# Optimization experiments

Hardware: AMD Instinct MI355X
Metric: run time of the kernel (lower is better)

The kernel has to match this reference:

```python
import jax, jax.numpy as jnp
import numpy as np
import math

VOCAB, E, CTX, DK, DH, H, HID, L = 50257, 768, 2048, 64, 64, 12, 3072, 2
B, S = 2, 2048
NEG_INF = -1e30


def _pos_encoding(seq_len, dim):
    pos = jnp.arange(seq_len, dtype=jnp.float32)[:, None]
    i = jnp.arange(dim, dtype=jnp.float32)[None, :]
    angle = pos / jnp.power(10000.0, 2.0 * i / dim)
    return jnp.where(jnp.arange(dim)[None, :] % 2 == 0, jnp.sin(angle), jnp.cos(angle))


def _layernorm(x, scale, bias, eps=1e-5):
    mu = jnp.mean(x, axis=-1, keepdims=True)
    var = jnp.var(x, axis=-1, keepdims=True)
    return (x - mu) * jax.lax.rsqrt(var + eps) * scale + bias


def setup_inputs() -> dict:
    key = jax.random.key(0)
    ks = jax.random.split(key, 10)
    s = 0.02  # init scale for stability
    return {
        "tokens": jax.random.randint(ks[0], (B, S), 0, VOCAB),
        "emb": jax.random.normal(ks[1], (VOCAB, E), jnp.float32) * s,
        "ln1_s": jnp.ones((L, E), jnp.float32),
        "ln1_b": jnp.zeros((L, E), jnp.float32),
        "Wq": jax.random.normal(ks[2], (L, H, E, DK), jnp.float32) * s,
        "bq": jnp.zeros((L, H, DK), jnp.float32),
        "Wk": jax.random.normal(ks[3], (L, H, E, DK), jnp.float32) * s,
        "bk": jnp.zeros((L, H, DK), jnp.float32),
        "Wv": jax.random.normal(ks[4], (L, H, E, DH), jnp.float32) * s,
        "bv": jnp.zeros((L, H, DH), jnp.float32),
        "ln2_s": jnp.ones((L, E), jnp.float32),
        "ln2_b": jnp.zeros((L, E), jnp.float32),
        "W1": jax.random.normal(ks[5], (L, E, HID), jnp.float32) * s,
        "b1": jnp.zeros((L, HID), jnp.float32),
        "W2": jax.random.normal(ks[6], (L, HID, E), jnp.float32) * s,
        "b2": jnp.zeros((L, E), jnp.float32),
        "Wout": jax.random.normal(ks[7], (E, VOCAB), jnp.float32) * s,
        "bout": jnp.zeros((VOCAB,), jnp.float32),
    }


def reference(tokens, emb, ln1_s, ln1_b, Wq, bq, Wk, bk, Wv, bv, ln2_s, ln2_b, W1, b1, W2, b2, Wout, bout):
    seq = tokens.shape[1]
    x = emb[tokens] + _pos_encoding(seq, E)  # [B,S,E]
    causal = jnp.triu(jnp.full((seq, seq), NEG_INF, jnp.float32), k=1)
    for l in range(Wq.shape[0]):
        # pre-norm on attention input; note residual adds to the NORMALIZED h (faithful to original)
        h = _layernorm(x, ln1_s[l], ln1_b[l])
        q = jnp.einsum('bse,hed->bhsd', h, Wq[l]) + bq[l][None, :, None, :]
        k = jnp.einsum('bse,hed->bhsd', h, Wk[l]) + bk[l][None, :, None, :]
        v = jnp.einsum('bse,hed->bhsd', h, Wv[l]) + bv[l][None, :, None, :]
        scores = jnp.einsum('bhsd,bhtd->bhst', q, k) / math.sqrt(DK) + causal
        w = jax.nn.softmax(scores, axis=-1)  # [B,H,S,S]
        o = jnp.einsum('bhst,bhtd->bhsd', w, v)  # [B,H,S,DH]
        o = jnp.transpose(o, (0, 2, 1, 3)).reshape(o.shape[0], seq, H * DH)  # concat heads
        x = h + o
        h2 = _layernorm(x, ln2_s[l], ln2_b[l])
        x = h2 + jnp.einsum('bsf,fe->bse', jax.nn.relu(jnp.einsum('bse,ef->bsf', h2, W1[l]) + b1[l]), W2[l]) + b2[l]
    logits = jnp.einsum('bse,ev->bsv', x, Wout) + bout  # training-mode output
    return logits
```

## Files before the change

kernel.cpp:

```cpp
#include <hip/hip_runtime.h>
#include <stdint.h>

#define DEV static __device__ __forceinline__

typedef unsigned short u16;
typedef __attribute__((ext_vector_type(8))) short short8;
typedef __attribute__((ext_vector_type(4))) float f32x4;

#define B_     2
#define S_     2048
#define E_     768
#define H_     12
#define L_     2
#define HID_   3072
#define VOCAB_ 50257
#define VPAD_  50304
#define M_     4096
#define NQKV_  2304

DEV u16 f2bf(float f) {
  union { float f; unsigned u; } x; x.f = f;
  unsigned r = x.u + 0x7fffu + ((x.u >> 16) & 1u);
  return (u16)(r >> 16);
}

DEV void gload16(const void* g, void* lds) {
  __builtin_amdgcn_global_load_lds(
      (const __attribute__((address_space(1))) unsigned int*)g,
      (__attribute__((address_space(3))) unsigned int*)lds, 16, 0, 0);
}

__global__ __launch_bounds__(256) void k_transp(
    const float* __restrict__ in, u16* __restrict__ out,
    int R, int Cin, long long ib1, long long ib2, long long ob1, long long ob2, int zdiv)
{
  __shared__ float t[32][33];
  const int z = blockIdx.z;
  const float* ib = in  + (size_t)(z / zdiv) * ib1 + (size_t)(z % zdiv) * ib2;
  u16*         ob = out + (size_t)(z / zdiv) * ob1 + (size_t)(z % zdiv) * ob2;
  const int c0 = blockIdx.x * 32, r0 = blockIdx.y * 32;
  const int tx = threadIdx.x, ty = threadIdx.y;
#pragma unroll
  for (int i = 0; i < 4; i++) {
    const int c = c0 + tx, r = r0 + ty + i * 8;
    t[ty + i * 8][tx] = (c < Cin) ? ib[(size_t)r * Cin + c] : 0.f;
  }
  __syncthreads();
#pragma unroll
  for (int i = 0; i < 4; i++) {
    const int orow = c0 + ty + i * 8;
    ob[(size_t)orow * R + r0 + tx] = f2bf(t[tx][ty + i * 8]);
  }
}

__global__ __launch_bounds__(256) void k_pack_bias(
    const float* __restrict__ bq, const float* __restrict__ bk,
    const float* __restrict__ bv, float* __restrict__ bqkv)
{
  const int i = blockIdx.x * 256 + threadIdx.x;
  if (i >= L_ * NQKV_) return;
  const int l = i / NQKV_, n = i % NQKV_;
  const float* s = (n < 768) ? bq : (n < 1536) ? bk : bv;
  bqkv[i] = s[l * 768 + (n % 768)];
}

__global__ __launch_bounds__(256) void k_embed(
    const int* __restrict__ tok, const float* __restrict__ emb, float* __restrict__ x)
{
  const int idx = blockIdx.x * 256 + threadIdx.x;
  const int e = idx % E_;
  const int row = idx / E_;
  const int s = row & (S_ - 1);
  const int t = tok[row];
  const float ang = (float)s * expf((float)e * (-2.0f / 768.f) * 9.210340371976184f);
  const float pe = (e & 1) ? cosf(ang) : sinf(ang);
  x[idx] = emb[(size_t)t * E_ + e] + pe;
}

__global__ __launch_bounds__(256) void k_ln(
    const float* __restrict__ xin, const float* __restrict__ sc,
    const float* __restrict__ bi, float* __restrict__ hout, u16* __restrict__ hb)
{
  const int row  = blockIdx.x * 4 + (threadIdx.x >> 6);
  const int lane = threadIdx.x & 63;
  const float* xr = xin + (size_t)row * E_;
  float v[12];
  float s = 0.f;
#pragma unroll
  for (int i = 0; i < 12; i++) { v[i] = xr[i * 64 + lane]; s += v[i]; }
#pragma unroll
  for (int o = 1; o < 64; o <<= 1) s += __shfl_xor(s, o);
  const float mu = s * (1.f / 768.f);
  float s2 = 0.f;
#pragma unroll
  for (int i = 0; i < 12; i++) { const float d = v[i] - mu; s2 += d * d; }
#pragma unroll
  for (int o = 1; o < 64; o <<= 1) s2 += __shfl_xor(s2, o);
  const float rs = rsqrtf(s2 * (1.f / 768.f) + 1e-5f);
#pragma unroll
  for (int i = 0; i < 12; i++) {
    const int c = i * 64 + lane;
    const float ov = (v[i] - mu) * rs * sc[c] + bi[c];
    hout[(size_t)row * E_ + c] = ov;
    hb[(size_t)row * E_ + c]   = f2bf(ov);
  }
}

__global__ __launch_bounds__(256) void k_f2b(
    const float* __restrict__ in, u16* __restrict__ o, int n)
{
  const int i = blockIdx.x * 256 + threadIdx.x;
  if (i < n) o[i] = f2bf(in[i]);
}

template <int EPI>
__global__ __launch_bounds__(256) void k_gemm(
    const u16* __restrict__ A, const u16* __restrict__ Bt,
    const float* __restrict__ bias, const float* __restrict__ res,
    void* __restrict__ outp, int Mm, int Nn, int Kk, int nreal)
{
  __shared__ __align__(16) u16 As[128 * 32];
  __shared__ __align__(16) u16 Bs[128 * 32];
  const int tid  = threadIdx.x;
  const int lane = tid & 63;
  const int wid  = tid >> 6;
  const int wr = wid >> 1, wc = wid & 1;
  const int m0 = blockIdx.y * 128, n0 = blockIdx.x * 128;

  const u16* Ab = A  + (size_t)m0 * Kk;
  const u16* Bb = Bt + (size_t)n0 * Kk;

  f32x4 acc[4][4];
#pragma unroll
  for (int i = 0; i < 4; i++)
#pragma unroll
    for (int j = 0; j < 4; j++) acc[i][j] = (f32x4){0.f, 0.f, 0.f, 0.f};

  const int c0 = tid, c1 = 256 + tid;
  const int a0row = c0 >> 2, a0k = (c0 & 3) * 8;
  const int a1row = c1 >> 2, a1k = (c1 & 3) * 8;
  const int nk = Kk >> 5;
  const int kg = (lane >> 4) * 8;
  const int arow = wr * 64 + (lane & 15);
  const int brow = wc * 64 + (lane & 15);

  for (int kt = 0; kt < nk; ++kt) {
    const int kof = kt * 32;
    __syncthreads();
    gload16(Ab + (size_t)a0row * Kk + kof + a0k, &As[c0 * 8]);
    gload16(Ab + (size_t)a1row * Kk + kof + a1k, &As[c1 * 8]);
    gload16(Bb + (size_t)a0row * Kk + kof + a0k, &Bs[c0 * 8]);
    gload16(Bb + (size_t)a1row * Kk + kof + a1k, &Bs[c1 * 8]);
    asm volatile("s_waitcnt vmcnt(0)" ::: "memory");
    __syncthreads();
    short8 af[4], bf[4];
#pragma unroll
    for (int i = 0; i < 4; i++) af[i] = *(const short8*)&As[(arow + i * 16) * 32 + kg];
#pragma unroll
    for (int i = 0; i < 4; i++) bf[i] = *(const short8*)&Bs[(brow + i * 16) * 32 + kg];
#pragma unroll
    for (int mi = 0; mi < 4; mi++)
#pragma unroll
      for (int ni = 0; ni < 4; ni++)
        acc[mi][ni] = __builtin_amdgcn_mfma_f32_16x16x32_bf16(af[mi], bf[ni], acc[mi][ni], 0, 0, 0);
  }

  const int colg = lane & 15;
  const int rowg = (lane >> 4) * 4;
#pragma unroll
  for (int mi = 0; mi < 4; mi++) {
#pragma unroll
    for (int ni = 0; ni < 4; ni++) {
      const int col = n0 + wc * 64 + ni * 16 + colg;
      const float bb = (EPI == 3 && col >= nreal) ? 0.f : bias[col];
#pragma unroll
      for (int r = 0; r < 4; r++) {
        const int row = m0 + wr * 64 + mi * 16 + rowg + r;
        float v = acc[mi][ni][r] + bb;
        if (EPI == 0)      ((u16*)outp)[(size_t)row * Nn + col] = f2bf(v);
        else if (EPI == 1) ((u16*)outp)[(size_t)row * Nn + col] = f2bf(fmaxf(v, 0.f));
        else if (EPI == 2) ((float*)outp)[(size_t)row * Nn + col] = v + res[(size_t)row * Nn + col];
        else { if (col < nreal) ((float*)outp)[(size_t)row * nreal + col] = v; }
      }
    }
  }
}

__global__ __launch_bounds__(256) void k_attn(
    const u16* __restrict__ qkv, const float* __restrict__ h, float* __restrict__ x)
{
  const int tid = threadIdx.x, lane = tid & 63, wid = tid >> 6;
  const int bh = blockIdx.y, b = bh / H_, hh = bh % H_;
  const int q0 = blockIdx.x * 64;
  const int qw = q0 + wid * 16;

  __shared__ __align__(16) u16 Ks[32 * 72];
  __shared__ __align__(16) u16 Vt[64 * 40];
  __shared__ __align__(16) u16 Ps[4][16 * 40];

  const size_t rowbase = (size_t)b * S_;
  const u16* qb = qkv + rowbase * NQKV_ + hh * 64;
  const u16* kb = qb + 768;
  const u16* vb = qb + 1536;

  const int l15 = lane & 15;
  const int kg  = (lane >> 4) * 8;

  short8 qf0, qf1;
  {
    const u16* g = qb + (size_t)(qw + l15) * NQKV_ + kg;
    qf0 = *(const short8*)g;
    qf1 = *(const short8*)(g + 32);
  }

  f32x4 ov[4];
#pragma unroll
  for (int i = 0; i < 4; i++) ov[i] = (f32x4){0.f, 0.f, 0.f, 0.f};
  float mr[4], lr[4];
#pragma unroll
  for (int r = 0; r < 4; r++) { mr[r] = -1e30f; lr[r] = 0.f; }

  const int srow = tid >> 3, sc8 = (tid & 7) * 8;
  const int nkt = q0 / 32 + 2;
  for (int kt = 0; kt < nkt; ++kt) {
    __syncthreads();
    {
      const size_t gr = (size_t)(kt * 32 + srow) * NQKV_;
      const uint4 kd = *(const uint4*)(kb + gr + sc8);
      *(uint4*)&Ks[srow * 72 + sc8] = kd;
      const uint4 vd = *(const uint4*)(vb + gr + sc8);
      const u16* ve = (const u16*)&vd;
#pragma unroll
      for (int j = 0; j < 8; j++) Vt[(sc8 + j) * 40 + srow] = ve[j];
    }
    __syncthreads();
    if (kt * 32 <= qw + 15) {
      f32x4 s0 = (f32x4){0.f, 0.f, 0.f, 0.f}, s1 = (f32x4){0.f, 0.f, 0.f, 0.f};
      const short8 k00 = *(const short8*)&Ks[l15 * 72 + kg];
      const short8 k01 = *(const short8*)&Ks[l15 * 72 + 32 + kg];
      const short8 k10 = *(const short8*)&Ks[(16 + l15) * 72 + kg];
      const short8 k11 = *(const short8*)&Ks[(16 + l15) * 72 + 32 + kg];
      s0 = __builtin_amdgcn_mfma_f32_16x16x32_bf16(qf0, k00, s0, 0, 0, 0);
      s0 = __builtin_amdgcn_mfma_f32_16x16x32_bf16(qf1, k01, s0, 0, 0, 0);
      s1 = __builtin_amdgcn_mfma_f32_16x16x32_bf16(qf0, k10, s1, 0, 0, 0);
      s1 = __builtin_amdgcn_mfma_f32_16x16x32_bf16(qf1, k11, s1, 0, 0, 0);

      const int qrow0 = qw + (lane >> 4) * 4;
      const int kc0 = kt * 32 + l15, kc1 = kc0 + 16;
      float p0[4], p1[4], mt[4];
#pragma unroll
      for (int r = 0; r < 4; r++) {
        const int qr = qrow0 + r;
        p0[r] = (kc0 <= qr) ? s0[r] * 0.125f : -1e30f;
        p1[r] = (kc1 <= qr) ? s1[r] * 0.125f : -1e30f;
        mt[r] = fmaxf(p0[r], p1[r]);
      }
#pragma unroll
      for (int r = 0; r < 4; r++) {
#pragma unroll
        for (int off = 1; off < 16; off <<= 1) mt[r] = fmaxf(mt[r], __shfl_xor(mt[r], off));
      }
      float al[4];
#pragma unroll
      for (int r = 0; r < 4; r++) {
        const float mn = fmaxf(mr[r], mt[r]);
        al[r] = __expf(mr[r] - mn);
        mr[r] = mn;
        p0[r] = __expf(p0[r] - mn);
        p1[r] = __expf(p1[r] - mn);
      }
      float ps[4];
#pragma unroll
      for (int r = 0; r < 4; r++) ps[r] = p0[r] + p1[r];
#pragma unroll
      for (int r = 0; r < 4; r++) {
#pragma unroll
        for (int off = 1; off < 16; off <<= 1) ps[r] += __shfl_xor(ps[r], off);
        lr[r] = lr[r] * al[r] + ps[r];
      }
#pragma unroll
      for (int dt = 0; dt < 4; dt++)
#pragma unroll
        for (int r = 0; r < 4; r++) ov[dt][r] *= al[r];

      u16* pw = &Ps[wid][0];
#pragma unroll
      for (int r = 0; r < 4; r++) {
        const int pr = (lane >> 4) * 4 + r;
        pw[pr * 40 + l15]      = f2bf(p0[r]);
        pw[pr * 40 + 16 + l15] = f2bf(p1[r]);
      }
      const short8 pa = *(const short8*)&pw[l15 * 40 + kg];
#pragma unroll
      for (int dt = 0; dt < 4; dt++) {
        const short8 vf = *(const short8*)&Vt[(dt * 16 + l15) * 40 + kg];
        ov[dt] = __builtin_amdgcn_mfma_f32_16x16x32_bf16(pa, vf, ov[dt], 0, 0, 0);
      }
    }
  }
#pragma unroll
  for (int dt = 0; dt < 4; dt++) {
#pragma unroll
    for (int r = 0; r < 4; r++) {
      const int qr = qw + (lane >> 4) * 4 + r;
      const int col = hh * 64 + dt * 16 + l15;
      const size_t idx = (rowbase + qr) * (size_t)E_ + col;
      x[idx] = h[idx] + ov[dt][r] / lr[r];
    }
  }
}

extern "C" void kernel_launch(void* const* d_in, const int* in_sizes, int n_in,
                              void* d_out, int out_size, void* d_ws, size_t ws_size,
                              hipStream_t stream)
{
  const int*   tok  = (const int*)  d_in[0];
  const float* emb  = (const float*)d_in[1];
  const float* ln1s = (const float*)d_in[2];
  const float* ln1b = (const float*)d_in[3];
  const float* Wq   = (const float*)d_in[4];
  const float* bq   = (const float*)d_in[5];
  const float* Wk   = (const float*)d_in[6];
  const float* bk   = (const float*)d_in[7];
  const float* Wv   = (const float*)d_in[8];
  const float* bv   = (const float*)d_in[9];
  const float* ln2s = (const float*)d_in[10];
  const float* ln2b = (const float*)d_in[11];
  const float* W1   = (const float*)d_in[12];
  const float* b1   = (const float*)d_in[13];
  const float* W2   = (const float*)d_in[14];
  const float* b2   = (const float*)d_in[15];
  const float* Wo   = (const float*)d_in[16];
  const float* bo   = (const float*)d_in[17];
  float* out = (float*)d_out;

  char* p = (char*)d_ws;
  float* xf    = (float*)p; p += (size_t)M_ * E_ * 4;
  float* hf    = (float*)p; p += (size_t)M_ * E_ * 4;
  u16*   hb    = (u16*)p;   p += (size_t)M_ * E_ * 2;
  u16*   xb    = (u16*)p;   p += (size_t)M_ * E_ * 2;
  u16*   midb  = (u16*)p;   p += (size_t)M_ * HID_ * 2;
  u16*   qkvb  = (u16*)p;   p += (size_t)M_ * NQKV_ * 2;
  u16*   Wqkvt = (u16*)p;   p += (size_t)L_ * NQKV_ * E_ * 2;
  u16*   W1t   = (u16*)p;   p += (size_t)L_ * HID_ * E_ * 2;
  u16*   W2t   = (u16*)p;   p += (size_t)L_ * E_ * HID_ * 2;
  u16*   Wot   = (u16*)p;   p += (size_t)VPAD_ * E_ * 2;
  float* bqkv  = (float*)p; p += (size_t)L_ * NQKV_ * 4;

  const dim3 tb32(32, 8, 1);
  k_transp<<<dim3(HID_ / 32, E_ / 32, L_), tb32, 0, stream>>>(
      W1, W1t, E_, HID_, (long long)E_ * HID_, 0, (long long)HID_ * E_, 0, 1);
  k_transp<<<dim3(E_ / 32, HID_ / 32, L_), tb32, 0, stream>>>(
      W2, W2t, HID_, E_, (long long)HID_ * E_, 0, (long long)E_ * HID_, 0, 1);
  k_transp<<<dim3(VPAD_ / 32, E_ / 32, 1), tb32, 0, stream>>>(
      Wo, Wot, E_, VOCAB_, 0, 0, 0, 0, 1);
  k_transp<<<dim3(2, E_ / 32, L_ * H_), tb32, 0, stream>>>(
      Wq, Wqkvt, E_, 64, (long long)H_ * E_ * 64, (long long)E_ * 64,
      (long long)NQKV_ * E_, 64LL * E_, H_);
  k_transp<<<dim3(2, E_ / 32, L_ * H_), tb32, 0, stream>>>(
      Wk, Wqkvt + 768 * E_, E_, 64, (long long)H_ * E_ * 64, (long long)E_ * 64,
      (long long)NQKV_ * E_, 64LL * E_, H_);
  k_transp<<<dim3(2, E_ / 32, L_ * H_), tb32, 0, stream>>>(
      Wv, Wqkvt + 1536 * E_, E_, 64, (long long)H_ * E_ * 64, (long long)E_ * 64,
      (long long)NQKV_ * E_, 64LL * E_, H_);
  k_pack_bias<<<18, 256, 0, stream>>>(bq, bk, bv, bqkv);
  k_embed<<<(M_ * E_) / 256, 256, 0, stream>>>(tok, emb, xf);

  for (int l = 0; l < L_; ++l) {
    k_ln<<<M_ / 4, 256, 0, stream>>>(xf, ln1s + l * E_, ln1b + l * E_, hf, hb);
    k_gemm<0><<<dim3(NQKV_ / 128, M_ / 128), 256, 0, stream>>>(
        hb, Wqkvt + (size_t)l * NQKV_ * E_, bqkv + l * NQKV_, nullptr, qkvb, M_, NQKV_, E_, 0);
    k_attn<<<dim3(S_ / 64, B_ * H_), 256, 0, stream>>>(qkvb, hf, xf);
    k_ln<<<M_ / 4, 256, 0, stream>>>(xf, ln2s + l * E_, ln2b + l * E_, hf, hb);
    k_gemm<1><<<dim3(HID_ / 128, M_ / 128), 256, 0, stream>>>(
        hb, W1t + (size_t)l * HID_ * E_, b1 + l * HID_, nullptr, midb, M_, HID_, E_, 0);
    k_gemm<2><<<dim3(E_ / 128, M_ / 128), 256, 0, stream>>>(
        midb, W2t + (size_t)l * E_ * HID_, b2 + l * E_, hf, xf, M_, E_, HID_, 0);
  }
  k_f2b<<<(M_ * E_) / 256, 256, 0, stream>>>(xf, xb, M_ * E_);
  k_gemm<3><<<dim3(VPAD_ / 128, M_ / 128), 256, 0, stream>>>(
      xb, Wot, bo, nullptr, out, M_, VPAD_, E_, VOCAB_);
}
```

Baseline: 1.357 ms.

## Add 256x256-tile 512-thread GEMM with 4-stage async LDS pipeline for wide projections

Introduces a new GEMM kernel with 256x256 output tiles, 8 waves, XOR-swizzled LDS, a 4-deep global_load_lds ring buffer with explicit vmcnt waits, and XCD-aware block remapping. It is used for the QKV, FFN1 and vocabulary projections. The vocabulary padding is raised to a multiple of 256 to fit the new tile. The aim is more data reuse per tile and better overlap of loads with MFMA, at the cost of high register use and one workgroup per CU. The QKV grid of 144 blocks may leave some CUs idle.

```diff
diff --git a/kernel.cpp b/kernel.cpp
--- a/kernel.cpp
+++ b/kernel.cpp
@@ -14,7 +14,7 @@
 #define L_     2
 #define HID_   3072
 #define VOCAB_ 50257
-#define VPAD_  50304
+#define VPAD_  50432
 #define M_     4096
 #define NQKV_  2304
 
@@ -172,7 +172,7 @@
 #pragma unroll
     for (int ni = 0; ni < 4; ni++) {
       const int col = n0 + wc * 64 + ni * 16 + colg;
-      const float bb = (EPI == 3 && col >= nreal) ? 0.f : bias[col];
+      const float bb = bias[col];
 #pragma unroll
       for (int r = 0; r < 4; r++) {
         const int row = m0 + wr * 64 + mi * 16 + rowg + r;
@@ -180,6 +180,112 @@
         if (EPI == 0)      ((u16*)outp)[(size_t)row * Nn + col] = f2bf(v);
         else if (EPI == 1) ((u16*)outp)[(size_t)row * Nn + col] = f2bf(fmaxf(v, 0.f));
         else if (EPI == 2) ((float*)outp)[(size_t)row * Nn + col] = v + res[(size_t)row * Nn + col];
+      }
+    }
+  }
+}
+
+template <int EPI>
+__global__ __launch_bounds__(512, 1) void k_gemm8(
+    const u16* __restrict__ A, const u16* __restrict__ Bt,
+    const float* __restrict__ bias, void* __restrict__ outp,
+    int Nn, int Kk, int nreal)
+{
+  __shared__ __align__(16) u16 As[4][256 * 32];
+  __shared__ __align__(16) u16 Bs[4][256 * 32];
+
+  const int nwg = gridDim.x, cpx = nwg >> 3;
+  int wg = blockIdx.x;
+  wg = (wg & 7) * cpx + (wg >> 3);
+  const int mi = wg & 15, ni = wg >> 4;
+  const int m0 = mi * 256, n0 = ni * 256;
+
+  const int tid = threadIdx.x;
+  const int lane = tid & 63;
+  const int w = tid >> 6;
+  const int wr = w >> 2, wcn = w & 3;
+
+  const u16* Ab = A  + (size_t)m0 * Kk;
+  const u16* Bb = Bt + (size_t)n0 * Kk;
+
+  const int srow = lane >> 2;
+  const int sslot = ((lane & 3) ^ ((lane >> 3) & 3)) * 8;
+  const size_t sA0 = (size_t)(w * 16 + srow) * Kk + sslot;
+  const size_t sA1 = (size_t)((w + 8) * 16 + srow) * Kk + sslot;
+
+  const int l15 = lane & 15, ks = lane >> 4;
+  const int ra0 = wr * 128 + l15;
+  const int aoffb = ra0 * 32 + ((ks ^ ((ra0 >> 1) & 3)) * 8);
+  const int rb0 = wcn * 64 + l15;
+  const int boffb = rb0 * 32 + ((ks ^ ((rb0 >> 1) & 3)) * 8);
+
+  f32x4 acc[8][4];
+#pragma unroll
+  for (int i = 0; i < 8; i++)
+#pragma unroll
+    for (int j = 0; j < 4; j++) acc[i][j] = (f32x4){0.f, 0.f, 0.f, 0.f};
+
+  const int nk = Kk >> 5;
+#pragma unroll
+  for (int t = 0; t < 3; ++t) {
+    const int ko = t * 32;
+    gload16(Ab + sA0 + ko, &As[t][w * 512]);
+    gload16(Ab + sA1 + ko, &As[t][(w + 8) * 512]);
+    gload16(Bb + sA0 + ko, &Bs[t][w * 512]);
+    gload16(Bb + sA1 + ko, &Bs[t][(w + 8) * 512]);
+  }
+
+  for (int t = 0; t < nk; ++t) {
+    const int cur = t & 3;
+    if (t + 3 < nk) {
+      const int nb = (t + 3) & 3;
+      const int ko = (t + 3) * 32;
+      gload16(Ab + sA0 + ko, &As[nb][w * 512]);
+      gload16(Ab + sA1 + ko, &As[nb][(w + 8) * 512]);
+      gload16(Bb + sA0 + ko, &Bs[nb][w * 512]);
+      gload16(Bb + sA1 + ko, &Bs[nb][(w + 8) * 512]);
+      asm volatile("s_waitcnt vmcnt(12)" ::: "memory");
+    } else if (t + 2 < nk) {
+      asm volatile("s_waitcnt vmcnt(8)" ::: "memory");
+    } else if (t + 1 < nk) {
+      asm volatile("s_waitcnt vmcnt(4)" ::: "memory");
+    } else {
+      asm volatile("s_waitcnt vmcnt(0)" ::: "memory");
+    }
+    __builtin_amdgcn_sched_barrier(0);
+    __builtin_amdgcn_s_barrier();
+    __builtin_amdgcn_sched_barrier(0);
+
+    short8 bfr[4];
+#pragma unroll
+    for (int fn = 0; fn < 4; fn++) bfr[fn] = *(const short8*)&Bs[cur][boffb + fn * 512];
+    __builtin_amdgcn_s_setprio(1);
+#pragma unroll
+    for (int fm = 0; fm < 8; fm++) {
+      const short8 af = *(const short8*)&As[cur][aoffb + fm * 512];
+#pragma unroll
+      for (int fn = 0; fn < 4; fn++)
+        acc[fm][fn] = __builtin_amdgcn_mfma_f32_16x16x32_bf16(af, bfr[fn], acc[fm][fn], 0, 0, 0);
+    }
+    __builtin_amdgcn_s_setprio(0);
+    __builtin_amdgcn_sched_barrier(0);
+    __builtin_amdgcn_s_barrier();
+    __builtin_amdgcn_sched_barrier(0);
+  }
+
+  const int rowg = (lane >> 4) * 4;
+#pragma unroll
+  for (int fn = 0; fn < 4; fn++) {
+    const int col = n0 + wcn * 64 + fn * 16 + l15;
+    const float bb = (EPI == 3 && col >= nreal) ? 0.f : bias[col];
+#pragma unroll
+    for (int fm = 0; fm < 8; fm++) {
+#pragma unroll
+      for (int r = 0; r < 4; r++) {
+        const int row = m0 + wr * 128 + fm * 16 + rowg + r;
+        float v = acc[fm][fn][r] + bb;
+        if (EPI == 0)      ((u16*)outp)[(size_t)row * Nn + col] = f2bf(v);
+        else if (EPI == 1) ((u16*)outp)[(size_t)row * Nn + col] = f2bf(fmaxf(v, 0.f));
         else { if (col < nreal) ((float*)outp)[(size_t)row * nreal + col] = v; }
       }
     }
@@ -368,16 +474,16 @@
 
   for (int l = 0; l < L_; ++l) {
     k_ln<<<M_ / 4, 256, 0, stream>>>(xf, ln1s + l * E_, ln1b + l * E_, hf, hb);
-    k_gemm<0><<<dim3(NQKV_ / 128, M_ / 128), 256, 0, stream>>>(
-        hb, Wqkvt + (size_t)l * NQKV_ * E_, bqkv + l * NQKV_, nullptr, qkvb, M_, NQKV_, E_, 0);
+    k_gemm8<0><<<16 * (NQKV_ / 256), 512, 0, stream>>>(
+        hb, Wqkvt + (size_t)l * NQKV_ * E_, bqkv + l * NQKV_, qkvb, NQKV_, E_, 0);
     k_attn<<<dim3(S_ / 64, B_ * H_), 256, 0, stream>>>(qkvb, hf, xf);
     k_ln<<<M_ / 4, 256, 0, stream>>>(xf, ln2s + l * E_, ln2b + l * E_, hf, hb);
-    k_gemm<1><<<dim3(HID_ / 128, M_ / 128), 256, 0, stream>>>(
-        hb, W1t + (size_t)l * HID_ * E_, b1 + l * HID_, nullptr, midb, M_, HID_, E_, 0);
+    k_gemm8<1><<<16 * (HID_ / 256), 512, 0, stream>>>(
+        hb, W1t + (size_t)l * HID_ * E_, b1 + l * HID_, midb, HID_, E_, 0);
     k_gemm<2><<<dim3(E_ / 128, M_ / 128), 256, 0, stream>>>(
         midb, W2t + (size_t)l * E_ * HID_, b2 + l * E_, hf, xf, M_, E_, HID_, 0);
   }
   k_f2b<<<(M_ * E_) / 256, 256, 0, stream>>>(xf, xb, M_ * E_);
-  k_gemm<3><<<dim3(VPAD_ / 128, M_ / 128), 256, 0, stream>>>(
-      xb, Wot, bo, nullptr, out, M_, VPAD_, E_, VOCAB_);
-}
+  k_gemm8<3><<<16 * (VPAD_ / 256), 512, 0, stream>>>(
+      xb, Wot, bo, out, VPAD_, E_, VOCAB_);
+}
```

New measurement: 1.662 ms. +22.5%, slower.

## Add 256x256 pipelined GEMM for vocab projection and fuse bf16 cast into FFN

Applied to the files above, without the earlier changes.

Replaces the 128x128 output-projection GEMM with a new 256x256-tile, 512-thread kernel. It uses K=64 double-buffered LDS staging through direct global-to-LDS loads, an XOR-swizzled LDS layout, MFMA priority hints and an XCD-aware block mapping. The vocab padding grows to a multiple of 256. The last layer's W2 GEMM now also writes the bf16 copy of x, which removes the separate f32-to-bf16 conversion kernel. The goal is higher MFMA utilisation and data reuse on the dominant logits GEMM, at the cost of a more fragile hand-scheduled pipeline, more padded columns, and fewer resident blocks from the larger LDS footprint.

```diff
diff --git a/kernel.cpp b/kernel.cpp
--- a/kernel.cpp
+++ b/kernel.cpp
@@ -14,7 +14,7 @@
 #define L_     2
 #define HID_   3072
 #define VOCAB_ 50257
-#define VPAD_  50304
+#define VPAD_  50432
 #define M_     4096
 #define NQKV_  2304
 
@@ -106,18 +106,11 @@
   }
 }
 
-__global__ __launch_bounds__(256) void k_f2b(
-    const float* __restrict__ in, u16* __restrict__ o, int n)
-{
-  const int i = blockIdx.x * 256 + threadIdx.x;
-  if (i < n) o[i] = f2bf(in[i]);
-}
-
 template <int EPI>
 __global__ __launch_bounds__(256) void k_gemm(
     const u16* __restrict__ A, const u16* __restrict__ Bt,
     const float* __restrict__ bias, const float* __restrict__ res,
-    void* __restrict__ outp, int Mm, int Nn, int Kk, int nreal)
+    void* __restrict__ outp, u16* __restrict__ out2, int Mm, int Nn, int Kk)
 {
   __shared__ __align__(16) u16 As[128 * 32];
   __shared__ __align__(16) u16 Bs[128 * 32];
@@ -172,7 +165,7 @@
 #pragma unroll
     for (int ni = 0; ni < 4; ni++) {
       const int col = n0 + wc * 64 + ni * 16 + colg;
-      const float bb = (EPI == 3 && col >= nreal) ? 0.f : bias[col];
+      const float bb = bias[col];
 #pragma unroll
       for (int r = 0; r < 4; r++) {
         const int row = m0 + wr * 64 + mi * 16 + rowg + r;
@@ -180,7 +173,136 @@
         if (EPI == 0)      ((u16*)outp)[(size_t)row * Nn + col] = f2bf(v);
         else if (EPI == 1) ((u16*)outp)[(size_t)row * Nn + col] = f2bf(fmaxf(v, 0.f));
         else if (EPI == 2) ((float*)outp)[(size_t)row * Nn + col] = v + res[(size_t)row * Nn + col];
-        else { if (col < nreal) ((float*)outp)[(size_t)row * nreal + col] = v; }
+        else if (EPI == 4) {
+          const float o = v + res[(size_t)row * Nn + col];
+          ((float*)outp)[(size_t)row * Nn + col] = o;
+          out2[(size_t)row * Nn + col] = f2bf(o);
+        }
+      }
+    }
+  }
+}
+
+__global__ __launch_bounds__(512, 2) void k_gemm256(
+    const u16* __restrict__ A, const u16* __restrict__ Bt,
+    const float* __restrict__ bias, float* __restrict__ out,
+    int Nn, int Kk, int nreal, int mpx)
+{
+  __shared__ __align__(16) u16 As[2][256 * 64];
+  __shared__ __align__(16) u16 Bs[2][256 * 64];
+
+  const int id = blockIdx.x;
+  const int xcd = id & 7;
+  const int j = id >> 3;
+  const int m0 = (xcd * mpx + (j % mpx)) * 256;
+  const int n0 = (j / mpx) * 256;
+
+  const int tid = threadIdx.x, lane = tid & 63, w = tid >> 6;
+  const int wr = w >> 2, wcn = w & 3;
+  const int l15 = lane & 15, ks = lane >> 4;
+
+  const u16* Ab = A  + (size_t)m0 * Kk;
+  const u16* Bb = Bt + (size_t)n0 * Kk;
+
+  const int srow  = lane >> 3;
+  const int sslot = ((lane & 7) ^ srow) * 8;
+  const int wrow  = w * 8;
+
+  f32x4 acc[8][4];
+#pragma unroll
+  for (int i = 0; i < 8; i++)
+#pragma unroll
+    for (int n = 0; n < 4; n++) acc[i][n] = (f32x4){0.f, 0.f, 0.f, 0.f};
+
+  const int nk = Kk >> 6;
+
+  auto stA = [&](int b, int R, int ko) {
+    gload16(Ab + (size_t)(R + wrow + srow) * Kk + ko + sslot,      &As[b][(R + wrow) * 64]);
+    gload16(Ab + (size_t)(R + 64 + wrow + srow) * Kk + ko + sslot, &As[b][(R + 64 + wrow) * 64]);
+  };
+  auto stB = [&](int b, int R, int ko) {
+    gload16(Bb + (size_t)(R + wrow + srow) * Kk + ko + sslot,      &Bs[b][(R + wrow) * 64]);
+    gload16(Bb + (size_t)(R + 64 + wrow + srow) * Kk + ko + sslot, &Bs[b][(R + 64 + wrow) * 64]);
+  };
+
+  short8 af[4], bf[4];
+  auto ldA = [&](int b, int fmh, int ksub) {
+#pragma unroll
+    for (int i = 0; i < 4; i++) {
+      const int r = wr * 128 + fmh * 64 + i * 16 + l15;
+      const int sl = ((ksub * 4 + ks) ^ (r & 7)) * 8;
+      af[i] = *(const short8*)&As[b][r * 64 + sl];
+    }
+  };
+  auto ldB = [&](int b, int ksub) {
+#pragma unroll
+    for (int n = 0; n < 4; n++) {
+      const int r = wcn * 64 + n * 16 + l15;
+      const int sl = ((ksub * 4 + ks) ^ (r & 7)) * 8;
+      bf[n] = *(const short8*)&Bs[b][r * 64 + sl];
+    }
+  };
+  auto mm = [&](int fmh) {
+    __builtin_amdgcn_s_setprio(1);
+#pragma unroll
+    for (int i = 0; i < 4; i++)
+#pragma unroll
+      for (int n = 0; n < 4; n++)
+        acc[fmh * 4 + i][n] =
+            __builtin_amdgcn_mfma_f32_16x16x32_bf16(af[i], bf[n], acc[fmh * 4 + i][n], 0, 0, 0);
+    __builtin_amdgcn_s_setprio(0);
+  };
+
+#define BAR_() do { __builtin_amdgcn_sched_barrier(0); __builtin_amdgcn_s_barrier(); \
+                    __builtin_amdgcn_sched_barrier(0); } while (0)
+#define LGKM_() do { asm volatile("s_waitcnt lgkmcnt(0)" ::: "memory"); \
+                     __builtin_amdgcn_sched_barrier(0); } while (0)
+
+  stA(0, 0, 0); stA(0, 128, 0); stB(0, 0, 0); stB(0, 128, 0);
+  if (nk > 1) {
+    stA(1, 0, 64); stA(1, 128, 64);
+    asm volatile("s_waitcnt vmcnt(4)" ::: "memory");
+  } else {
+    asm volatile("s_waitcnt vmcnt(0)" ::: "memory");
+  }
+  BAR_();
+
+  for (int t = 0; t < nk; ++t) {
+    const int cur = t & 1;
+    const int kon = (t + 1) << 6;
+    ldA(cur, 0, 0); ldB(cur, 0);
+    if (t + 1 < nk) stB(cur ^ 1, 0, kon);
+    BAR_(); LGKM_(); mm(0); BAR_();
+    ldA(cur, 1, 0);
+    if (t + 1 < nk) stB(cur ^ 1, 128, kon);
+    BAR_(); LGKM_(); mm(1); BAR_();
+    ldA(cur, 0, 1); ldB(cur, 1);
+    BAR_(); LGKM_(); mm(0); BAR_();
+    ldA(cur, 1, 1);
+    BAR_(); LGKM_(); mm(1); BAR_();
+    if (t + 2 < nk) {
+      const int kon2 = (t + 2) << 6;
+      stA(cur, 0, kon2); stA(cur, 128, kon2);
+      asm volatile("s_waitcnt vmcnt(4)" ::: "memory");
+    } else {
+      asm volatile("s_waitcnt vmcnt(0)" ::: "memory");
+    }
+    BAR_();
+  }
+#undef BAR_
+#undef LGKM_
+
+#pragma unroll
+  for (int fm = 0; fm < 8; fm++) {
+    const int row = m0 + wr * 128 + fm * 16 + ks * 4;
+#pragma unroll
+    for (int n = 0; n < 4; n++) {
+      const int col = n0 + wcn * 64 + n * 16 + l15;
+      if (col < nreal) {
+        const float bb = bias[col];
+#pragma unroll
+        for (int r = 0; r < 4; r++)
+          out[(size_t)(row + r) * nreal + col] = acc[fm][n][r] + bb;
       }
     }
   }
@@ -369,15 +491,21 @@
   for (int l = 0; l < L_; ++l) {
     k_ln<<<M_ / 4, 256, 0, stream>>>(xf, ln1s + l * E_, ln1b + l * E_, hf, hb);
     k_gemm<0><<<dim3(NQKV_ / 128, M_ / 128), 256, 0, stream>>>(
-        hb, Wqkvt + (size_t)l * NQKV_ * E_, bqkv + l * NQKV_, nullptr, qkvb, M_, NQKV_, E_, 0);
+        hb, Wqkvt + (size_t)l * NQKV_ * E_, bqkv + l * NQKV_, nullptr, qkvb, nullptr,
+        M_, NQKV_, E_);
     k_attn<<<dim3(S_ / 64, B_ * H_), 256, 0, stream>>>(qkvb, hf, xf);
     k_ln<<<M_ / 4, 256, 0, stream>>>(xf, ln2s + l * E_, ln2b + l * E_, hf, hb);
     k_gemm<1><<<dim3(HID_ / 128, M_ / 128), 256, 0, stream>>>(
-        hb, W1t + (size_t)l * HID_ * E_, b1 + l * HID_, nullptr, midb, M_, HID_, E_, 0);
-    k_gemm<2><<<dim3(E_ / 128, M_ / 128), 256, 0, stream>>>(
-        midb, W2t + (size_t)l * E_ * HID_, b2 + l * E_, hf, xf, M_, E_, HID_, 0);
-  }
-  k_f2b<<<(M_ * E_) / 256, 256, 0, stream>>>(xf, xb, M_ * E_);
-  k_gemm<3><<<dim3(VPAD_ / 128, M_ / 128), 256, 0, stream>>>(
-      xb, Wot, bo, nullptr, out, M_, VPAD_, E_, VOCAB_);
-}
+        hb, W1t + (size_t)l * HID_ * E_, b1 + l * HID_, nullptr, midb, nullptr,
+        M_, HID_, E_);
+    if (l == L_ - 1) {
+      k_gemm<4><<<dim3(E_ / 128, M_ / 128), 256, 0, stream>>>(
+          midb, W2t + (size_t)l * E_ * HID_, b2 + l * E_, hf, xf, xb, M_, E_, HID_);
+    } else {
+      k_gemm<2><<<dim3(E_ / 128, M_ / 128), 256, 0, stream>>>(
+          midb, W2t + (size_t)l * E_ * HID_, b2 + l * E_, hf, xf, nullptr, M_, E_, HID_);
+    }
+  }
+  k_gemm256<<<dim3(8 * 2 * (VPAD_ / 256)), 512, 0, stream>>>(
+      xb, Wot, bo, out, VPAD_, E_, VOCAB_, 2);
+}
```

Result: faster. 1.322 ms (-2.5%).
